# Performance work log

Measured on AMD Instinct MI355X. Metric: run time of the kernel, lower is better.

## Reference

```python
import jax, jax.numpy as jnp
import numpy as np

N, E, F = 32768, 131072, 32

# (l_in, l_edge, l_out, op_type) for each of the 12 active paths; index = row of W
PATHS = [
    (0, 0, 0, 'prod'), (0, 1, 1, 'prod'), (0, 2, 2, 'prod'),
    (1, 0, 1, 'prod'), (2, 0, 2, 'prod'),
    (1, 1, 0, 'dot'), (1, 1, 1, 'cross'), (1, 1, 2, 'outer'),
    (2, 1, 1, 'mat_vec'), (1, 2, 1, 'vec_mat'),
    (2, 2, 0, 'double_dot'), (2, 2, 2, 'mat_mul_sym'),
]


def setup_inputs() -> dict:
    key = jax.random.key(0)
    ks = jax.random.split(key, 8)
    return {
        'h0': jax.random.normal(ks[0], (N, F), jnp.float32),
        'h1': jax.random.normal(ks[1], (N, 3, F), jnp.float32),
        'h2': jax.random.normal(ks[2], (N, 3, 3, F), jnp.float32),
        'g0': jax.random.normal(ks[3], (E, F), jnp.float32),
        'g1': jax.random.normal(ks[4], (E, 3, F), jnp.float32),
        'g2': jax.random.normal(ks[5], (E, 3, 3, F), jnp.float32),
        'W': jax.random.normal(ks[6], (len(PATHS), F, F), jnp.float32) * (F ** -0.5),
        'src': jax.random.randint(ks[7], (E,), 0, N, jnp.int32).astype(jnp.int64),
    }


def _leibniz(h0, h1, h2, g0, g1, g2, W, src):
    inv_sqrt_f = h0.shape[-1] ** -0.5
    # gather source-node features once per l
    h = {0: h0[src], 1: h1[src], 2: h2[src]}
    g = {0: g0, 1: g1, 2: g2}
    eye = jnp.eye(3, dtype=h0.dtype)[None, :, :, None]  # [1,3,3,1]
    msgs = {0: [], 1: [], 2: []}
    for p, (li, le, lo, op) in enumerate(PATHS):
        # nn.Linear(F,F,bias=False): y = x @ W^T, applied on last (feature) axis
        ht = jnp.einsum('...f,gf->...g', h[li], W[p])
        geom = g[le]
        if op == 'prod':
            if li == 0 and le == 0:
                res = ht * geom
            elif li == 0 and le == 1:
                res = ht[:, None, :] * geom
            elif li == 0 and le == 2:
                res = ht[:, None, None, :] * geom
            elif li == 1 and le == 0:
                res = ht * geom[:, None, :]
            else:  # li == 2, le == 0
                res = ht * geom[:, None, None, :]
        elif op == 'dot':
            res = jnp.sum(ht * geom, axis=1)
        elif op == 'cross':
            res = jnp.cross(ht, geom, axisa=1, axisb=1, axisc=1)
        elif op == 'outer':
            outer = ht[:, :, None, :] * geom[:, None, :, :]  # [E,3,3,F]
            trace = jnp.einsum('eiif->ef', outer)
            res = outer - (1.0 / 3.0) * trace[:, None, None, :] * eye
        elif op == 'mat_vec':
            res = jnp.einsum('eijf,ejf->eif', ht, geom)
        elif op == 'vec_mat':
            res = jnp.einsum('eif,eijf->ejf', ht, geom)
        elif op == 'double_dot':
            res = jnp.sum(ht * geom, axis=(1, 2))
        else:  # mat_mul_sym
            raw = jnp.einsum('eikf,ekjf->eijf', ht, geom)
            sym = 0.5 * (raw + jnp.swapaxes(raw, 1, 2))
            trace = jnp.einsum('eiif->ef', sym)
            res = sym - (1.0 / 3.0) * trace[:, None, None, :] * eye
        msgs[lo].append(res * inv_sqrt_f)
    return tuple(sum(msgs[l]) for l in (0, 1, 2))


def reference(h0, h1, h2, g0, g1, g2, W, src):
    return _leibniz(h0, h1, h2, g0, g1, g2, W, src)
```

## Files before the change

### kernel.cpp

```cpp
#include <hip/hip_runtime.h>

typedef float f32x4 __attribute__((ext_vector_type(4)));
typedef __bf16 bf16x8 __attribute__((ext_vector_type(8)));

constexpr float INV_SQRT_F = 0.17677669529663687f;

__device__ __forceinline__ f32x4 mfma16(bf16x8 a, bf16x8 b) {
  const f32x4 z = {0.f, 0.f, 0.f, 0.f};
  return __builtin_amdgcn_mfma_f32_16x16x32_bf16(a, b, z, 0, 0, 0);
}

__device__ __forceinline__ bf16x8 load_frag8(const float* __restrict__ p) {
  f32x4 u = *reinterpret_cast<const f32x4*>(p);
  f32x4 v = *reinterpret_cast<const f32x4*>(p + 4);
  bf16x8 r;
  r[0] = (__bf16)u[0]; r[1] = (__bf16)u[1]; r[2] = (__bf16)u[2]; r[3] = (__bf16)u[3];
  r[4] = (__bf16)v[0]; r[5] = (__bf16)v[1]; r[6] = (__bf16)v[2]; r[7] = (__bf16)v[3];
  return r;
}

__global__ __launch_bounds__(256, 2)
void leibniz_fused(const float* __restrict__ h0, const float* __restrict__ h1,
                   const float* __restrict__ h2, const float* __restrict__ g0,
                   const float* __restrict__ g1, const float* __restrict__ g2,
                   const float* __restrict__ Wg, const int* __restrict__ src,
                   float* __restrict__ out, int E)
{
  __shared__ bf16x8 wlds[12 * 2 * 4 * 16];

  for (int c = threadIdx.x; c < 12 * 2 * 4 * 16; c += 256) {
    const int gl = c & 15;
    const int qq = (c >> 4) & 3;
    const int hf = (c >> 6) & 1;
    const int p  = c >> 7;
    const float* wp = Wg + (p * 32 + hf * 16 + gl) * 32 + qq * 8;
    bf16x8 f;
#pragma unroll
    for (int j = 0; j < 8; ++j) f[j] = (__bf16)(wp[j] * INV_SQRT_F);
    wlds[c] = f;
  }
  __syncthreads();

  const int lane = threadIdx.x & 63;
  const int wid  = threadIdx.x >> 6;
  const int eidx = lane & 15;
  const int q    = lane >> 4;
  int e0 = (blockIdx.x * 4 + wid) * 16;
  if (e0 > E - 16) e0 = E - 16;

  const int node = src[e0 + eidx];
  const int k0 = q * 8;

  const bf16x8 b0 = load_frag8(h0 + node * 32 + k0);
  bf16x8 b1[3];
#pragma unroll
  for (int s = 0; s < 3; ++s) b1[s] = load_frag8(h1 + node * 96 + s * 32 + k0);
  bf16x8 b2[9];
#pragma unroll
  for (int s = 0; s < 9; ++s) b2[s] = load_frag8(h2 + node * 288 + s * 32 + k0);

  const int e   = e0 + eidx;
  const int col = q * 4;
  const float* g0p = g0 + e * 32 + col;
  const float* g1p = g1 + (long long)e * 96 + col;
  const float* g2p = g2 + (long long)e * 288 + col;
  float* o0p = out + (long long)e * 32 + col;
  float* o1p = out + (long long)E * 32 + (long long)e * 96 + col;
  float* o2p = out + (long long)E * 128 + (long long)e * 288 + col;

  const f32x4 z4 = {0.f, 0.f, 0.f, 0.f};
  f32x4 acc0[2] = {z4, z4};
  f32x4 acc1[3][2];
  f32x4 acc2[9][2];
#pragma unroll
  for (int s = 0; s < 3; ++s) { acc1[s][0] = z4; acc1[s][1] = z4; }
#pragma unroll
  for (int s = 0; s < 9; ++s) { acc2[s][0] = z4; acc2[s][1] = z4; }

#define WFRAG(P, H) (wlds[(((P) * 2 + (H)) * 4 + q) * 16 + eidx])

  {
    f32x4 gv[2];
    gv[0] = *reinterpret_cast<const f32x4*>(g0p);
    gv[1] = *reinterpret_cast<const f32x4*>(g0p + 16);
#pragma unroll
    for (int h = 0; h < 2; ++h) {
      acc0[h] += mfma16(WFRAG(0, h), b0) * gv[h];
      const bf16x8 w3 = WFRAG(3, h);
#pragma unroll
      for (int s = 0; s < 3; ++s) acc1[s][h] += mfma16(w3, b1[s]) * gv[h];
      const bf16x8 w4 = WFRAG(4, h);
#pragma unroll
      for (int s = 0; s < 9; ++s) acc2[s][h] += mfma16(w4, b2[s]) * gv[h];
    }
  }

  {
    f32x4 gv[3][2];
#pragma unroll
    for (int s = 0; s < 3; ++s) {
      gv[s][0] = *reinterpret_cast<const f32x4*>(g1p + s * 32);
      gv[s][1] = *reinterpret_cast<const f32x4*>(g1p + s * 32 + 16);
    }
#pragma unroll
    for (int h = 0; h < 2; ++h) {
      {
        const f32x4 t = mfma16(WFRAG(1, h), b0);
#pragma unroll
        for (int s = 0; s < 3; ++s) acc1[s][h] += t * gv[s][h];
      }
      {
        const bf16x8 w5 = WFRAG(5, h);
#pragma unroll
        for (int s = 0; s < 3; ++s) acc0[h] += mfma16(w5, b1[s]) * gv[s][h];
      }
      {
        const bf16x8 w6 = WFRAG(6, h);
        const f32x4 c0 = mfma16(w6, b1[0]);
        const f32x4 c1 = mfma16(w6, b1[1]);
        const f32x4 c2 = mfma16(w6, b1[2]);
        acc1[0][h] += c1 * gv[2][h] - c2 * gv[1][h];
        acc1[1][h] += c2 * gv[0][h] - c0 * gv[2][h];
        acc1[2][h] += c0 * gv[1][h] - c1 * gv[0][h];
      }
      {
        const bf16x8 w7 = WFRAG(7, h);
        const f32x4 o0 = mfma16(w7, b1[0]);
        const f32x4 o1 = mfma16(w7, b1[1]);
        const f32x4 o2 = mfma16(w7, b1[2]);
        const f32x4 tr3 = (o0 * gv[0][h] + o1 * gv[1][h] + o2 * gv[2][h]) * (1.f / 3.f);
        acc2[0][h] += o0 * gv[0][h] - tr3;
        acc2[1][h] += o0 * gv[1][h];
        acc2[2][h] += o0 * gv[2][h];
        acc2[3][h] += o1 * gv[0][h];
        acc2[4][h] += o1 * gv[1][h] - tr3;
        acc2[5][h] += o1 * gv[2][h];
        acc2[6][h] += o2 * gv[0][h];
        acc2[7][h] += o2 * gv[1][h];
        acc2[8][h] += o2 * gv[2][h] - tr3;
      }
      {
        const bf16x8 w8 = WFRAG(8, h);
#pragma unroll
        for (int i = 0; i < 3; ++i)
#pragma unroll
          for (int j = 0; j < 3; ++j)
            acc1[i][h] += mfma16(w8, b2[i * 3 + j]) * gv[j][h];
      }
    }
  }

  {
    f32x4 t2[2];
    t2[0] = mfma16(WFRAG(2, 0), b0);
    t2[1] = mfma16(WFRAG(2, 1), b0);
#pragma unroll
    for (int k = 0; k < 3; ++k) {
      f32x4 gk[3][2];
#pragma unroll
      for (int j = 0; j < 3; ++j) {
        gk[j][0] = *reinterpret_cast<const f32x4*>(g2p + (k * 3 + j) * 32);
        gk[j][1] = *reinterpret_cast<const f32x4*>(g2p + (k * 3 + j) * 32 + 16);
      }
#pragma unroll
      for (int h = 0; h < 2; ++h) {
#pragma unroll
        for (int j = 0; j < 3; ++j) acc2[k * 3 + j][h] += t2[h] * gk[j][h];
        {
          const f32x4 vk = mfma16(WFRAG(9, h), b1[k]);
#pragma unroll
          for (int j = 0; j < 3; ++j) acc1[j][h] += vk * gk[j][h];
        }
        {
          const bf16x8 w10 = WFRAG(10, h);
#pragma unroll
          for (int j = 0; j < 3; ++j) acc0[h] += mfma16(w10, b2[k * 3 + j]) * gk[j][h];
        }
        {
          const bf16x8 w11 = WFRAG(11, h);
          const f32x4 m0 = mfma16(w11, b2[0 * 3 + k]);
          const f32x4 m1 = mfma16(w11, b2[1 * 3 + k]);
          const f32x4 m2 = mfma16(w11, b2[2 * 3 + k]);
          const f32x4 tk3 = (m0 * gk[0][h] + m1 * gk[1][h] + m2 * gk[2][h]) * (1.f / 3.f);
          acc2[0][h] += m0 * gk[0][h] - tk3;
          acc2[4][h] += m1 * gk[1][h] - tk3;
          acc2[8][h] += m2 * gk[2][h] - tk3;
          const f32x4 s01 = (m0 * gk[1][h] + m1 * gk[0][h]) * 0.5f;
          acc2[1][h] += s01; acc2[3][h] += s01;
          const f32x4 s02 = (m0 * gk[2][h] + m2 * gk[0][h]) * 0.5f;
          acc2[2][h] += s02; acc2[6][h] += s02;
          const f32x4 s12 = (m1 * gk[2][h] + m2 * gk[1][h]) * 0.5f;
          acc2[5][h] += s12; acc2[7][h] += s12;
        }
      }
    }
  }

  *reinterpret_cast<f32x4*>(o0p)      = acc0[0];
  *reinterpret_cast<f32x4*>(o0p + 16) = acc0[1];
#pragma unroll
  for (int s = 0; s < 3; ++s) {
    *reinterpret_cast<f32x4*>(o1p + s * 32)      = acc1[s][0];
    *reinterpret_cast<f32x4*>(o1p + s * 32 + 16) = acc1[s][1];
  }
#pragma unroll
  for (int s = 0; s < 9; ++s) {
    *reinterpret_cast<f32x4*>(o2p + s * 32)      = acc2[s][0];
    *reinterpret_cast<f32x4*>(o2p + s * 32 + 16) = acc2[s][1];
  }
#undef WFRAG
}

extern "C" void kernel_launch(void* const* d_in, const int* in_sizes, int n_in,
                              void* d_out, int out_size, void* d_ws, size_t ws_size,
                              hipStream_t stream) {
  const float* h0 = (const float*)d_in[0];
  const float* h1 = (const float*)d_in[1];
  const float* h2 = (const float*)d_in[2];
  const float* g0 = (const float*)d_in[3];
  const float* g1 = (const float*)d_in[4];
  const float* g2 = (const float*)d_in[5];
  const float* Wg = (const float*)d_in[6];
  const int* src = (const int*)d_in[7];
  const int E = in_sizes[7];
  const int blocks = (E + 63) / 64;
  leibniz_fused<<<blocks, 256, 0, stream>>>(h0, h1, h2, g0, g1, g2, Wg, src,
                                            (float*)d_out, E);
}
```

Baseline: 131.1 us.

## Split output feature halves across wave pairs and prefetch edge geometry

Each 16-edge tile is now handled by two waves, each computing one 16-column half of the output features. This halves per-thread accumulators and raises the occupancy hint from 2 to 3 blocks per SIMD. Edge geometry loads for g0, g1 and g2 are issued earlier and double-buffered across the g2 rows, and s_barrier calls are added to keep sibling waves in step. In exchange, the gathered h fragments are loaded twice (once per wave) and the grid launches twice as many blocks, each also rebuilding the shared W tile.

```diff
diff --git a/kernel.cpp b/kernel.cpp
--- a/kernel.cpp
+++ b/kernel.cpp
@@ -19,7 +19,7 @@
   return r;
 }
 
-__global__ __launch_bounds__(256, 2)
+__global__ __launch_bounds__(256, 3)
 void leibniz_fused(const float* __restrict__ h0, const float* __restrict__ h1,
                    const float* __restrict__ h2, const float* __restrict__ g0,
                    const float* __restrict__ g1, const float* __restrict__ g2,
@@ -43,171 +43,170 @@
 
   const int lane = threadIdx.x & 63;
   const int wid  = threadIdx.x >> 6;
+  const int half = wid & 1;
+  const int tile = wid >> 1;
   const int eidx = lane & 15;
   const int q    = lane >> 4;
-  int e0 = (blockIdx.x * 4 + wid) * 16;
+  int e0 = (blockIdx.x * 2 + tile) * 16;
   if (e0 > E - 16) e0 = E - 16;
 
   const int node = src[e0 + eidx];
-  const int k0 = q * 8;
-
-  const bf16x8 b0 = load_frag8(h0 + node * 32 + k0);
-  bf16x8 b1[3];
-#pragma unroll
-  for (int s = 0; s < 3; ++s) b1[s] = load_frag8(h1 + node * 96 + s * 32 + k0);
-  bf16x8 b2[9];
-#pragma unroll
-  for (int s = 0; s < 9; ++s) b2[s] = load_frag8(h2 + node * 288 + s * 32 + k0);
 
   const int e   = e0 + eidx;
-  const int col = q * 4;
+  const int col = q * 4 + 16 * half;
   const float* g0p = g0 + e * 32 + col;
   const float* g1p = g1 + (long long)e * 96 + col;
   const float* g2p = g2 + (long long)e * 288 + col;
+
+  f32x4 gv0 = *reinterpret_cast<const f32x4*>(g0p);
+  f32x4 gv1[3];
+#pragma unroll
+  for (int s = 0; s < 3; ++s)
+    gv1[s] = *reinterpret_cast<const f32x4*>(g1p + s * 32);
+
+  const int k0 = q * 8;
+  const bf16x8 b0 = load_frag8(h0 + node * 32 + k0);
+  bf16x8 b1[3];
+#pragma unroll
+  for (int s = 0; s < 3; ++s) b1[s] = load_frag8(h1 + node * 96 + s * 32 + k0);
+  bf16x8 b2[9];
+#pragma unroll
+  for (int s = 0; s < 9; ++s) b2[s] = load_frag8(h2 + node * 288 + s * 32 + k0);
+
+  const f32x4 z4 = {0.f, 0.f, 0.f, 0.f};
+  f32x4 acc0 = z4;
+  f32x4 acc1[3] = {z4, z4, z4};
+  f32x4 acc2[9] = {z4, z4, z4, z4, z4, z4, z4, z4, z4};
+
+#define WFRAG(P) (wlds[(((P) * 2 + half) * 4 + q) * 16 + eidx])
+
+  {
+    acc0 += mfma16(WFRAG(0), b0) * gv0;
+    const bf16x8 w3 = WFRAG(3);
+#pragma unroll
+    for (int s = 0; s < 3; ++s) acc1[s] += mfma16(w3, b1[s]) * gv0;
+    const bf16x8 w4 = WFRAG(4);
+#pragma unroll
+    for (int s = 0; s < 9; ++s) acc2[s] += mfma16(w4, b2[s]) * gv0;
+  }
+
+  f32x4 gkA[3];
+#pragma unroll
+  for (int j = 0; j < 3; ++j)
+    gkA[j] = *reinterpret_cast<const f32x4*>(g2p + j * 32);
+
+  __builtin_amdgcn_s_barrier();
+
+  {
+    {
+      const f32x4 t = mfma16(WFRAG(1), b0);
+#pragma unroll
+      for (int s = 0; s < 3; ++s) acc1[s] += t * gv1[s];
+    }
+    {
+      const bf16x8 w5 = WFRAG(5);
+#pragma unroll
+      for (int s = 0; s < 3; ++s) acc0 += mfma16(w5, b1[s]) * gv1[s];
+    }
+    {
+      const bf16x8 w6 = WFRAG(6);
+      const f32x4 c0 = mfma16(w6, b1[0]);
+      const f32x4 c1 = mfma16(w6, b1[1]);
+      const f32x4 c2 = mfma16(w6, b1[2]);
+      acc1[0] += c1 * gv1[2] - c2 * gv1[1];
+      acc1[1] += c2 * gv1[0] - c0 * gv1[2];
+      acc1[2] += c0 * gv1[1] - c1 * gv1[0];
+    }
+    {
+      const bf16x8 w7 = WFRAG(7);
+      const f32x4 o0 = mfma16(w7, b1[0]);
+      const f32x4 o1 = mfma16(w7, b1[1]);
+      const f32x4 o2 = mfma16(w7, b1[2]);
+      const f32x4 tr3 = (o0 * gv1[0] + o1 * gv1[1] + o2 * gv1[2]) * (1.f / 3.f);
+      acc2[0] += o0 * gv1[0] - tr3;
+      acc2[1] += o0 * gv1[1];
+      acc2[2] += o0 * gv1[2];
+      acc2[3] += o1 * gv1[0];
+      acc2[4] += o1 * gv1[1] - tr3;
+      acc2[5] += o1 * gv1[2];
+      acc2[6] += o2 * gv1[0];
+      acc2[7] += o2 * gv1[1];
+      acc2[8] += o2 * gv1[2] - tr3;
+    }
+    {
+      const bf16x8 w8 = WFRAG(8);
+#pragma unroll
+      for (int i = 0; i < 3; ++i)
+#pragma unroll
+        for (int j = 0; j < 3; ++j)
+          acc1[i] += mfma16(w8, b2[i * 3 + j]) * gv1[j];
+    }
+  }
+
+  f32x4 gkB[3];
+#pragma unroll
+  for (int j = 0; j < 3; ++j)
+    gkB[j] = *reinterpret_cast<const f32x4*>(g2p + (3 + j) * 32);
+
+  f32x4 t2 = mfma16(WFRAG(2), b0);
+
+#define G2ROW_COMPUTE(K, GK)                                                   \
+  {                                                                            \
+    _Pragma("unroll")                                                          \
+    for (int j = 0; j < 3; ++j) acc2[(K) * 3 + j] += t2 * GK[j];               \
+    {                                                                          \
+      const f32x4 vk = mfma16(WFRAG(9), b1[(K)]);                              \
+      _Pragma("unroll")                                                        \
+      for (int j = 0; j < 3; ++j) acc1[j] += vk * GK[j];                       \
+    }                                                                          \
+    {                                                                          \
+      const bf16x8 w10 = WFRAG(10);                                            \
+      _Pragma("unroll")                                                        \
+      for (int j = 0; j < 3; ++j)                                              \
+        acc0 += mfma16(w10, b2[(K) * 3 + j]) * GK[j];                          \
+    }                                                                          \
+    {                                                                          \
+      const bf16x8 w11 = WFRAG(11);                                            \
+      const f32x4 m0 = mfma16(w11, b2[0 * 3 + (K)]);                           \
+      const f32x4 m1 = mfma16(w11, b2[1 * 3 + (K)]);                           \
+      const f32x4 m2 = mfma16(w11, b2[2 * 3 + (K)]);                           \
+      const f32x4 tk3 = (m0 * GK[0] + m1 * GK[1] + m2 * GK[2]) * (1.f / 3.f);  \
+      acc2[0] += m0 * GK[0] - tk3;                                             \
+      acc2[4] += m1 * GK[1] - tk3;                                             \
+      acc2[8] += m2 * GK[2] - tk3;                                             \
+      const f32x4 s01 = (m0 * GK[1] + m1 * GK[0]) * 0.5f;                      \
+      acc2[1] += s01; acc2[3] += s01;                                          \
+      const f32x4 s02 = (m0 * GK[2] + m2 * GK[0]) * 0.5f;                      \
+      acc2[2] += s02; acc2[6] += s02;                                          \
+      const f32x4 s12 = (m1 * GK[2] + m2 * GK[1]) * 0.5f;                      \
+      acc2[5] += s12; acc2[7] += s12;                                          \
+    }                                                                          \
+  }
+
+  G2ROW_COMPUTE(0, gkA)
+
+#pragma unroll
+  for (int j = 0; j < 3; ++j)
+    gkA[j] = *reinterpret_cast<const f32x4*>(g2p + (6 + j) * 32);
+
+  G2ROW_COMPUTE(1, gkB)
+  G2ROW_COMPUTE(2, gkA)
+
+#undef G2ROW_COMPUTE
+
+  __builtin_amdgcn_s_barrier();
+
   float* o0p = out + (long long)e * 32 + col;
   float* o1p = out + (long long)E * 32 + (long long)e * 96 + col;
   float* o2p = out + (long long)E * 128 + (long long)e * 288 + col;
 
-  const f32x4 z4 = {0.f, 0.f, 0.f, 0.f};
-  f32x4 acc0[2] = {z4, z4};
-  f32x4 acc1[3][2];
-  f32x4 acc2[9][2];
-#pragma unroll
-  for (int s = 0; s < 3; ++s) { acc1[s][0] = z4; acc1[s][1] = z4; }
-#pragma unroll
-  for (int s = 0; s < 9; ++s) { acc2[s][0] = z4; acc2[s][1] = z4; }
-
-#define WFRAG(P, H) (wlds[(((P) * 2 + (H)) * 4 + q) * 16 + eidx])
-
-  {
-    f32x4 gv[2];
-    gv[0] = *reinterpret_cast<const f32x4*>(g0p);
-    gv[1] = *reinterpret_cast<const f32x4*>(g0p + 16);
-#pragma unroll
-    for (int h = 0; h < 2; ++h) {
-      acc0[h] += mfma16(WFRAG(0, h), b0) * gv[h];
-      const bf16x8 w3 = WFRAG(3, h);
-#pragma unroll
-      for (int s = 0; s < 3; ++s) acc1[s][h] += mfma16(w3, b1[s]) * gv[h];
-      const bf16x8 w4 = WFRAG(4, h);
-#pragma unroll
-      for (int s = 0; s < 9; ++s) acc2[s][h] += mfma16(w4, b2[s]) * gv[h];
-    }
-  }
-
-  {
-    f32x4 gv[3][2];
-#pragma unroll
-    for (int s = 0; s < 3; ++s) {
-      gv[s][0] = *reinterpret_cast<const f32x4*>(g1p + s * 32);
-      gv[s][1] = *reinterpret_cast<const f32x4*>(g1p + s * 32 + 16);
-    }
-#pragma unroll
-    for (int h = 0; h < 2; ++h) {
-      {
-        const f32x4 t = mfma16(WFRAG(1, h), b0);
-#pragma unroll
-        for (int s = 0; s < 3; ++s) acc1[s][h] += t * gv[s][h];
-      }
-      {
-        const bf16x8 w5 = WFRAG(5, h);
-#pragma unroll
-        for (int s = 0; s < 3; ++s) acc0[h] += mfma16(w5, b1[s]) * gv[s][h];
-      }
-      {
-        const bf16x8 w6 = WFRAG(6, h);
-        const f32x4 c0 = mfma16(w6, b1[0]);
-        const f32x4 c1 = mfma16(w6, b1[1]);
-        const f32x4 c2 = mfma16(w6, b1[2]);
-        acc1[0][h] += c1 * gv[2][h] - c2 * gv[1][h];
-        acc1[1][h] += c2 * gv[0][h] - c0 * gv[2][h];
-        acc1[2][h] += c0 * gv[1][h] - c1 * gv[0][h];
-      }
-      {
-        const bf16x8 w7 = WFRAG(7, h);
-        const f32x4 o0 = mfma16(w7, b1[0]);
-        const f32x4 o1 = mfma16(w7, b1[1]);
-        const f32x4 o2 = mfma16(w7, b1[2]);
-        const f32x4 tr3 = (o0 * gv[0][h] + o1 * gv[1][h] + o2 * gv[2][h]) * (1.f / 3.f);
-        acc2[0][h] += o0 * gv[0][h] - tr3;
-        acc2[1][h] += o0 * gv[1][h];
-        acc2[2][h] += o0 * gv[2][h];
-        acc2[3][h] += o1 * gv[0][h];
-        acc2[4][h] += o1 * gv[1][h] - tr3;
-        acc2[5][h] += o1 * gv[2][h];
-        acc2[6][h] += o2 * gv[0][h];
-        acc2[7][h] += o2 * gv[1][h];
-        acc2[8][h] += o2 * gv[2][h] - tr3;
-      }
-      {
-        const bf16x8 w8 = WFRAG(8, h);
-#pragma unroll
-        for (int i = 0; i < 3; ++i)
-#pragma unroll
-          for (int j = 0; j < 3; ++j)
-            acc1[i][h] += mfma16(w8, b2[i * 3 + j]) * gv[j][h];
-      }
-    }
-  }
-
-  {
-    f32x4 t2[2];
-    t2[0] = mfma16(WFRAG(2, 0), b0);
-    t2[1] = mfma16(WFRAG(2, 1), b0);
-#pragma unroll
-    for (int k = 0; k < 3; ++k) {
-      f32x4 gk[3][2];
-#pragma unroll
-      for (int j = 0; j < 3; ++j) {
-        gk[j][0] = *reinterpret_cast<const f32x4*>(g2p + (k * 3 + j) * 32);
-        gk[j][1] = *reinterpret_cast<const f32x4*>(g2p + (k * 3 + j) * 32 + 16);
-      }
-#pragma unroll
-      for (int h = 0; h < 2; ++h) {
-#pragma unroll
-        for (int j = 0; j < 3; ++j) acc2[k * 3 + j][h] += t2[h] * gk[j][h];
-        {
-          const f32x4 vk = mfma16(WFRAG(9, h), b1[k]);
-#pragma unroll
-          for (int j = 0; j < 3; ++j) acc1[j][h] += vk * gk[j][h];
-        }
-        {
-          const bf16x8 w10 = WFRAG(10, h);
-#pragma unroll
-          for (int j = 0; j < 3; ++j) acc0[h] += mfma16(w10, b2[k * 3 + j]) * gk[j][h];
-        }
-        {
-          const bf16x8 w11 = WFRAG(11, h);
-          const f32x4 m0 = mfma16(w11, b2[0 * 3 + k]);
-          const f32x4 m1 = mfma16(w11, b2[1 * 3 + k]);
-          const f32x4 m2 = mfma16(w11, b2[2 * 3 + k]);
-          const f32x4 tk3 = (m0 * gk[0][h] + m1 * gk[1][h] + m2 * gk[2][h]) * (1.f / 3.f);
-          acc2[0][h] += m0 * gk[0][h] - tk3;
-          acc2[4][h] += m1 * gk[1][h] - tk3;
-          acc2[8][h] += m2 * gk[2][h] - tk3;
-          const f32x4 s01 = (m0 * gk[1][h] + m1 * gk[0][h]) * 0.5f;
-          acc2[1][h] += s01; acc2[3][h] += s01;
-          const f32x4 s02 = (m0 * gk[2][h] + m2 * gk[0][h]) * 0.5f;
-          acc2[2][h] += s02; acc2[6][h] += s02;
-          const f32x4 s12 = (m1 * gk[2][h] + m2 * gk[1][h]) * 0.5f;
-          acc2[5][h] += s12; acc2[7][h] += s12;
-        }
-      }
-    }
-  }
-
-  *reinterpret_cast<f32x4*>(o0p)      = acc0[0];
-  *reinterpret_cast<f32x4*>(o0p + 16) = acc0[1];
-#pragma unroll
-  for (int s = 0; s < 3; ++s) {
-    *reinterpret_cast<f32x4*>(o1p + s * 32)      = acc1[s][0];
-    *reinterpret_cast<f32x4*>(o1p + s * 32 + 16) = acc1[s][1];
-  }
-#pragma unroll
-  for (int s = 0; s < 9; ++s) {
-    *reinterpret_cast<f32x4*>(o2p + s * 32)      = acc2[s][0];
-    *reinterpret_cast<f32x4*>(o2p + s * 32 + 16) = acc2[s][1];
-  }
+  *reinterpret_cast<f32x4*>(o0p) = acc0;
+#pragma unroll
+  for (int s = 0; s < 3; ++s)
+    *reinterpret_cast<f32x4*>(o1p + s * 32) = acc1[s];
+#pragma unroll
+  for (int s = 0; s < 9; ++s)
+    *reinterpret_cast<f32x4*>(o2p + s * 32) = acc2[s];
 #undef WFRAG
 }
 
@@ -223,7 +222,7 @@
   const float* Wg = (const float*)d_in[6];
   const int* src = (const int*)d_in[7];
   const int E = in_sizes[7];
-  const int blocks = (E + 63) / 64;
+  const int blocks = (E + 31) / 32;
   leibniz_fused<<<blocks, 256, 0, stream>>>(h0, h1, h2, g0, g1, g2, Wg, src,
                                             (float*)d_out, E);
 }
```

After: 168.6 us. 28.7% more time.
